# Kernel optimization log

Measured on AMD Instinct MI355X. Metric: run time of the kernel, lower is better.

## Reference

```python
import jax, jax.numpy as jnp
import numpy as np

NL, D, Di, N, R, K, V, NH = 24, 768, 1536, 16, 48, 4, 50280, 12
BATCH, SEQ = 4, 256


def setup_inputs():
    key = jax.random.key(0)
    it = iter(jax.random.split(key, 48))
    g = lambda shape, s=0.02: jax.random.normal(next(it), shape, jnp.float32) * s
    inp = {
        "question_ids": jax.random.randint(next(it), (BATCH, SEQ), 0, V),
        "question_mask": jnp.ones((BATCH, SEQ), jnp.int32),
        "answer_ids": jax.random.randint(next(it), (BATCH, SEQ), 0, V),
        "answer_mask": jnp.ones((BATCH, SEQ), jnp.int32),
        "embed": g((V, D)),
        "norm_w": jnp.ones((NL, D)),
        "in_proj_w": g((NL, 2 * Di, D)),
        "conv_w": g((NL, Di, K), 0.1),
        "conv_b": jnp.zeros((NL, Di)),
        "x_proj_w": g((NL, R + 2 * N, Di)),
        "dt_proj_w": g((NL, Di, R)),
        "dt_proj_b": g((NL, Di), 0.5) - 4.0,
        "A_log": jnp.log(jnp.broadcast_to(jnp.arange(1, N + 1, dtype=jnp.float32), (NL, Di, N))) + 0.0,
        "D_p": jnp.ones((NL, Di)),
        "out_proj_w": g((NL, D, Di)),
        "norm_f": jnp.ones((D,)),
        "ln1_w": jnp.ones((D,)), "ln1_b": jnp.zeros((D,)),
        "qkv_w": g((3 * D, D)), "qkv_b": jnp.zeros((3 * D,)),
        "attn_out_w": g((D, D)), "attn_out_b": jnp.zeros((D,)),
        "ln2_w": jnp.ones((D,)), "ln2_b": jnp.zeros((D,)),
        "ff1_w": g((4 * D, D)), "ff1_b": jnp.zeros((4 * D,)),
        "ff2_w": g((D, 4 * D)), "ff2_b": jnp.zeros((D,)),
        "C_w": g((1, N)), "proj_out_w": g((D, Di)),
        "B_w": g((N, 1)), "proj_in_w": g((Di, D), 0.002),
    }
    return inp


def _rms(x, w, eps=1e-5):
    return x * jax.lax.rsqrt(jnp.mean(x * x, axis=-1, keepdims=True) + eps) * w


def _ln(x, w, b, eps=1e-5):
    m = jnp.mean(x, axis=-1, keepdims=True)
    v = jnp.var(x, axis=-1, keepdims=True)
    return (x - m) * jax.lax.rsqrt(v + eps) * w + b


def _mamba_block(h, layer, init_state):
    nw, ipw, cw, cb, xpw, dpw, dpb, alog, dp, opw = layer
    x_in = _rms(h, nw)
    xz = jnp.einsum('bld,ed->ble', x_in, ipw)  # (B,L,2*Di)
    x, z = jnp.split(xz, 2, axis=-1)
    L = x.shape[1]
    xp = jnp.pad(x, ((0, 0), (K - 1, 0), (0, 0)))  # causal depthwise conv, kernel K
    x = sum(xp[:, k:k + L, :] * cw[:, k] for k in range(K)) + cb
    x = jax.nn.silu(x)
    dbl = jnp.einsum('bld,ed->ble', x, xpw)
    dt, Bm, Cm = dbl[..., :R], dbl[..., R:R + N], dbl[..., R + N:]
    delta = jax.nn.softplus(jnp.einsum('blr,dr->bld', dt, dpw) + dpb)  # (B,L,Di)
    A = -jnp.exp(alog)  # (Di,N)

    def step(hs, t):  # selective scan, carry (B,Di,N)
        d_t, x_t, B_t, C_t = t
        hs = jnp.exp(d_t[..., None] * A) * hs + (d_t * x_t)[..., None] * B_t[:, None, :]
        return hs, jnp.einsum('bdn,bn->bd', hs, C_t)

    xs = tuple(jnp.moveaxis(a, 1, 0) for a in (delta, x, Bm, Cm))
    last, ys = jax.lax.scan(step, init_state, xs)
    y = jnp.moveaxis(ys, 0, 1) + x * dp
    y = y * jax.nn.silu(z)
    return h + jnp.einsum('bld,od->blo', y, opw), last


def _backbone(ids, mask, embed, mamba_params, norm_f, init_states):
    h = embed[ids] * mask[..., None].astype(embed.dtype)
    block = jax.checkpoint(_mamba_block)  # remat per layer: bounds bwd memory

    def layer_step(carry, xs):
        *layer, st = xs
        return block(carry, tuple(layer), st)

    h, lasts = jax.lax.scan(layer_step, h, mamba_params + (init_states,))
    h = _rms(h, norm_f)
    return jnp.einsum('bld,vd->blv', h, embed), lasts  # tied lm head


def _tf_layer(x, ln1_w, ln1_b, qkv_w, qkv_b, attn_out_w, attn_out_b, ln2_w, ln2_b, ff1_w, ff1_b, ff2_w, ff2_b):
    B, S, _ = x.shape
    hd = D // NH
    y = _ln(x, ln1_w, ln1_b)  # norm_first pre-LN
    q, k, v = jnp.split(y @ qkv_w.T + qkv_b, 3, axis=-1)
    q = q.reshape(B, S, NH, hd); k = k.reshape(B, S, NH, hd); v = v.reshape(B, S, NH, hd)
    att = jax.nn.softmax(jnp.einsum('bqhd,bkhd->bhqk', q, k) / jnp.sqrt(jnp.float32(hd)), axis=-1)
    o = jnp.einsum('bhqk,bkhd->bqhd', att, v).reshape(B, S, D)
    x = x + o @ attn_out_w.T + attn_out_b
    y = _ln(x, ln2_w, ln2_b)
    return x + jax.nn.gelu(y @ ff1_w.T + ff1_b, approximate=False) @ ff2_w.T + ff2_b


def _refine(states, C_w, proj_out_w, B_w, proj_in_w, tf_params):
    # states: (B, NL, Di, N); 12-step recurrent state refinement
    for _ in range(12):
        d = jnp.einsum('bsdn,n->bsd', states, C_w[0])  # C: Linear(16,1), squeeze(-1)
        d = jnp.einsum('bsd,od->bso', d, proj_out_w)   # 1536 -> 768
        d = _tf_layer(d, *tf_params)
        d = jnp.einsum('bso,do->bsd', d, proj_in_w)    # 768 -> 1536
        states = states + d[..., None] * B_w[:, 0]     # B: Linear(1,16)
    return states


def reference(question_ids, question_mask, answer_ids, answer_mask, embed, norm_w, in_proj_w, conv_w, conv_b, x_proj_w, dt_proj_w, dt_proj_b, A_log, D_p, out_proj_w, norm_f, ln1_w, ln1_b, qkv_w, qkv_b, attn_out_w, attn_out_b, ln2_w, ln2_b, ff1_w, ff1_b, ff2_w, ff2_b, C_w, proj_out_w, B_w, proj_in_w):
    mamba_params = (norm_w, in_proj_w, conv_w, conv_b, x_proj_w, dt_proj_w, dt_proj_b, A_log, D_p, out_proj_w)
    tf_params = (ln1_w, ln1_b, qkv_w, qkv_b, attn_out_w, attn_out_b, ln2_w, ln2_b, ff1_w, ff1_b, ff2_w, ff2_b)
    Bsz = question_ids.shape[0]
    zeros = jnp.zeros((NL, Bsz, Di, N), embed.dtype)
    _, lasts = _backbone(question_ids, question_mask, embed, mamba_params, norm_f, zeros)
    states = jnp.moveaxis(lasts, 0, 1)  # torch.stack(states, dim=1): (B, NL, Di, N)
    states = _refine(states, C_w, proj_out_w, B_w, proj_in_w, tf_params)
    logits, _ = _backbone(answer_ids, answer_mask, embed, mamba_params, norm_f, jnp.moveaxis(states, 0, 1))
    return logits
```

## Files before the change

### kernel.cpp

```cpp
#include <hip/hip_runtime.h>
#include <math.h>

namespace {

constexpr int kNL = 24, kD = 768, kDi = 1536, kN = 16, kR = 48, kK = 4, kV = 50280, kNH = 12;
constexpr int kB = 4, kS = 256;
constexpr int kMtok = kB * kS;
constexpr int kMref = kB * kNL;
constexpr int kVp = 50304;
constexpr int kKa = 3840;

using bf16x8   = __attribute__((ext_vector_type(8))) short;
using f32x4    = __attribute__((ext_vector_type(4))) float;
using ushort8v = __attribute__((ext_vector_type(8))) unsigned short;

__device__ __forceinline__ float siluf(float x) { return x / (1.f + __expf(-x)); }

__device__ __forceinline__ ushort f2b(float f) {
    union { float f; unsigned u; } v; v.f = f;
    unsigned u = v.u;
    unsigned r = (u + 0x7FFFu + ((u >> 16) & 1u)) >> 16;
    return (ushort)r;
}
__device__ __forceinline__ float b2f(ushort u) {
    union { unsigned u; float f; } v; v.u = (unsigned)u << 16; return v.f;
}

#define GLOAD_LDS(g, l) \
    __builtin_amdgcn_global_load_lds((const __attribute__((address_space(1))) void*)(g), \
                                     (__attribute__((address_space(3))) void*)(l), 16, 0, 0)

template <int BM, int BN, int BIAS, int ACT, int RES, int OUTMODE, int PIPE, int SSQ = 0, int SWZ = 0>
__global__ __launch_bounds__(256, (PIPE == 3 ? 3 : 2)) void gemm_bf16(
    const ushort* __restrict__ A, int lda,
    const ushort* __restrict__ B, int ldb,
    float* __restrict__ C, int ldc,
    ushort* __restrict__ Cbf, int ldcb,
    float* __restrict__ C2,
    const float* __restrict__ bias,
    const float* __restrict__ aux,
    const float* __restrict__ aux2,
    int M, int N, int K)
{
// ... 155 lines not shown
            for (int q = 0; q < 4; ++q) {
                rsq[i][q] += __shfl_xor(rsq[i][q], 1, 16);
                rsq[i][q] += __shfl_xor(rsq[i][q], 2, 16);
                rsq[i][q] += __shfl_xor(rsq[i][q], 4, 16);
                rsq[i][q] += __shfl_xor(rsq[i][q], 8, 16);
            }
        float* red = (float*)&As[0][0];
        __syncthreads();
        if ((lane & 15) == 0) {
#pragma unroll
            for (int i = 0; i < MI; ++i)
#pragma unroll
                for (int q = 0; q < 4; ++q) {
                    int rl = (wave >> 1) * 32 + i * 16 + (lane >> 4) * 4 + q;
                    red[(wave & 1) * 64 + rl] = rsq[i][q];
                }
        }
        __syncthreads();
        if (tid < 64) C2[(size_t)blockIdx.x * kMtok + m0 + tid] = red[tid] + red[64 + tid];
    }
}

template <int BM, int BN, int BIAS, int ACT, int RES, int OUTMODE, int PIPE, int SSQ = 0, int SWZ = 0>
static void gemm(const ushort* A, int lda, const ushort* B, int ldb,
                 float* C, int ldc, ushort* Cb, int ldcb, float* C2,
                 const float* bias, const float* aux, int M, int N, int K, hipStream_t s,
                 const float* aux2 = nullptr)
{
    dim3 g((N + BN - 1) / BN, (M + BM - 1) / BM);
    gemm_bf16<BM, BN, BIAS, ACT, RES, OUTMODE, PIPE, SSQ, SWZ><<<g, dim3(256), 0, s>>>(
        A, lda, B, ldb, C, ldc, Cb, ldcb, C2, bias, aux, aux2, M, N, K);
}

__global__ __launch_bounds__(256, 4) void gemm_rms(
    const float* __restrict__ hbuf, const float* __restrict__ ssq,
    const float* __restrict__ nw,
    const ushort* __restrict__ B, int ldb,
    ushort* __restrict__ Xbf, ushort* __restrict__ zTb,
    int M, int N, int K)
{
    constexpr int MI = 2, NJ = 2, BCH = 2;
    __shared__ ushort As[2][64 * 64];
    __shared__ ushort Bs[2][64 * 64];
    const int tid  = threadIdx.x;
    const int lane = tid & 63;
    const int wave = tid >> 6;
    const int m0 = blockIdx.y * 64;
    const int n0 = blockIdx.x * 64;
    const int wr = (wave >> 1) * 32;
    const int wc = (wave & 1) * 32;

    f32x4 acc[MI][NJ];
#pragma unroll
    for (int i = 0; i < MI; ++i)
#pragma unroll
        for (int j = 0; j < NJ; ++j) acc[i][j] = f32x4{0.f, 0.f, 0.f, 0.f};

    const int srow = lane >> 3;
    const int scol = ((lane & 7) ^ srow) * 8;
    const ushort* gB[BCH];
#pragma unroll
    for (int g = 0; g < BCH; ++g)
        gB[g] = B + (size_t)(n0 + (g * 4 + wave) * 8 + srow) * ldb + scol;

    int arow[2];
    float rs[2];
#pragma unroll
    for (int g = 0; g < 2; ++g) {
        arow[g] = m0 + (g * 4 + wave) * 8 + srow;
        float s = 0.f;
#pragma unroll
        for (int c = 0; c < 12; ++c) s += ssq[c * kMtok + arow[g]];
        rs[g] = rsqrtf(s * (1.f / 768.f) + 1e-5f);
    }

    const int frow = lane & 15;
    const int kh   = lane >> 4;
    const int nt   = K >> 6;

    float4 av[2][2], wv[2];
    auto loadA = [&](int t) {
        int k = t * 64 + scol;
        wv[0] = *(const float4*)&nw[k];
        wv[1] = *(const float4*)&nw[k + 4];
#pragma unroll
        for (int g = 0; g < 2; ++g) {
            av[g][0] = *(const float4*)&hbuf[(size_t)arow[g] * K + k];
            av[g][1] = *(const float4*)&hbuf[(size_t)arow[g] * K + k + 4];
        }
    };
    auto writeA = [&](int buf) {
#pragma unroll
        for (int g = 0; g < 2; ++g) {
            ushort8v o;
            o[0] = f2b(av[g][0].x * rs[g] * wv[0].x);
            o[1] = f2b(av[g][0].y * rs[g] * wv[0].y);
            o[2] = f2b(av[g][0].z * rs[g] * wv[0].z);
            o[3] = f2b(av[g][0].w * rs[g] * wv[0].w);
            o[4] = f2b(av[g][1].x * rs[g] * wv[1].x);
            o[5] = f2b(av[g][1].y * rs[g] * wv[1].y);
            o[6] = f2b(av[g][1].z * rs[g] * wv[1].z);
            o[7] = f2b(av[g][1].w * rs[g] * wv[1].w);
            *(ushort8v*)&As[buf][(g * 4 + wave) * 512 + lane * 8] = o;
        }
    };
    auto stageB = [&](int t, int buf) {
#pragma unroll
        for (int g = 0; g < BCH; ++g) GLOAD_LDS(gB[g] + t * 64, &Bs[buf][(g * 4 + wave) * 512]);
    };
    auto compute = [&](int buf) {
#pragma unroll
        for (int s = 0; s < 2; ++s) {
            bf16x8 fa[MI], fb[NJ];
#pragma unroll
            for (int i = 0; i < MI; ++i) {
                int r = wr + i * 16 + frow;
                int slot = (s * 4 + kh) ^ (r & 7);
                fa[i] = *(const bf16x8*)&As[buf][r * 64 + slot * 8];
            }
#pragma unroll
            for (int j = 0; j < NJ; ++j) {
                int r = wc + j * 16 + frow;
                int slot = (s * 4 + kh) ^ (r & 7);
                fb[j] = *(const bf16x8*)&Bs[buf][r * 64 + slot * 8];
            }
#pragma unroll
            for (int i = 0; i < MI; ++i)
#pragma unroll
                for (int j = 0; j < NJ; ++j)
                    acc[i][j] = __builtin_amdgcn_mfma_f32_16x16x32_bf16(fa[i], fb[j], acc[i][j], 0, 0, 0);
        }
    };

    loadA(0);
    stageB(0, 0);
    writeA(0);
    __syncthreads();
    int cur = 0;
    for (int t = 0; t < nt; ++t) {
        if (t + 1 < nt) { loadA(t + 1); stageB(t + 1, cur ^ 1); }
        compute(cur);
        if (t + 1 < nt) writeA(cur ^ 1);
        __syncthreads();
        cur ^= 1;
    }

    const int ccol = lane & 15;
    const int crow = (lane >> 4) * 4;
#pragma unroll
    for (int i = 0; i < MI; ++i) {
#pragma unroll
        for (int j = 0; j < NJ; ++j) {
            int gn = n0 + wc + j * 16 + ccol;
#pragma unroll
            for (int q = 0; q < 4; ++q) {
                int gm = m0 + wr + i * 16 + crow + q;
                float v = acc[i][j][q];
                if (gn < kDi) Xbf[(size_t)gm * kDi + gn] = f2b(v);
                else zTb[(size_t)(gn - kDi) * kMtok + gm] = f2b(siluf(v));
            }
        }
    }
}

__global__ void cvt_kernel(const float* __restrict__ src, ushort* __restrict__ dst, int n) {
    int i = (blockIdx.x * 256 + threadIdx.x) * 4;
    if (i >= n) return;
    float4 v = *(const float4*)(src + i);
    ushort4 o; o.x = f2b(v.x); o.y = f2b(v.y); o.z = f2b(v.z); o.w = f2b(v.w);
    *(ushort4*)(dst + i) = o;
}

__global__ void cvt_xpw_kernel(const float* __restrict__ src, ushort* __restrict__ dst) {
    int i = (blockIdx.x * 256 + threadIdx.x) * 4;
    if (i >= 24 * 80 * 1536) return;
    int l = i / (80 * 1536), r = i - l * (80 * 1536);
    int row = r / 1536, col = r - row * 1536;
    float4 v = *(const float4*)(src + i);
    ushort4 o; o.x = f2b(v.x); o.y = f2b(v.y); o.z = f2b(v.z); o.w = f2b(v.w);
    *(ushort4*)(dst + ((size_t)(l * 128 + row)) * 1536 + col) = o;
}

__global__ void cvt_dpw_kernel(const float* __restrict__ src, ushort* __restrict__ dst) {
    int i = blockIdx.x * 256 + threadIdx.x;
    if (i >= 24 * 1536 * 64) return;
    int col = i & 63, row = i >> 6;
    dst[i] = (col < 48) ? f2b(src[(size_t)row * 48 + col]) : (ushort)0;
}

__global__ void cvt_ff2T_kernel(const float* __restrict__ src, ushort* __restrict__ dst) {
    int i = blockIdx.x * 256 + threadIdx.x;
    if (i >= 768 * 3072) return;
    int d = i / 3072, f = i - d * 3072;
    dst[(size_t)f * 768 + d] = f2b(src[i]);
}

__global__ void cvt_pi_kernel(const float* __restrict__ src, ushort* __restrict__ dst) {
    int i = blockIdx.x * 256 + threadIdx.x;
    if (i >= 1536 * 768) return;
    int o = i / 768, d = i - o * 768;
    dst[(size_t)o * kKa + d] = f2b(src[i]);
}

__global__ void pib_kernel(const float* __restrict__ piw, const float* __restrict__ ff2b,
                           float* __restrict__ bias2) {
    int o = blockIdx.x * 256 + threadIdx.x;
    if (o >= 1536) return;
    float s = 0.f;
    for (int d = 0; d < 768; ++d) s += piw[(size_t)o * 768 + d] * ff2b[d];
    bias2[o] = s;
}

__global__ void embed_kernel(const int* __restrict__ ids, const int* __restrict__ msk,
                             const float* __restrict__ embed, float* __restrict__ h,
                             float* __restrict__ ssq)
{
    int i = blockIdx.x * 256 + threadIdx.x;
    int row = i / kD, col = i - row * kD;
    float v = embed[(size_t)ids[row] * kD + col] * (float)msk[row];
    h[i] = v;
    float s = v * v;
    s += __shfl_xor(s, 1);  s += __shfl_xor(s, 2);  s += __shfl_xor(s, 4);
    s += __shfl_xor(s, 8);  s += __shfl_xor(s, 16); s += __shfl_xor(s, 32);
    if ((threadIdx.x & 63) == 0) ssq[(col >> 6) * kMtok + row] = s;
}

__global__ __launch_bounds__(256) void rms_kernel(const float* __restrict__ x,
                                                  const float* __restrict__ w,
                                                  ushort* __restrict__ out)
{
    __shared__ float red[256];
    int row = blockIdx.x, tid = threadIdx.x;
    const float* xr = x + (size_t)row * kD;
    float s = 0.f;
    for (int j = tid; j < kD; j += 256) { float v = xr[j]; s += v * v; }
    red[tid] = s; __syncthreads();
    for (int o = 128; o > 0; o >>= 1) { if (tid < o) red[tid] += red[tid + o]; __syncthreads(); }
    float rs = rsqrtf(red[0] / (float)kD + 1e-5f);
    for (int j = tid; j < kD; j += 256) out[(size_t)row * kD + j] = f2b(xr[j] * rs * w[j]);
}

__global__ __launch_bounds__(256) void ln_kernel(const float* __restrict__ x,
                                                 const float* __restrict__ w,
                                                 const float* __restrict__ b,
                                                 ushort* __restrict__ out)
{
    __shared__ float r1[256], r2[256];
    int row = blockIdx.x, tid = threadIdx.x;
    const float* xr = x + (size_t)row * kD;
    float s = 0.f, s2 = 0.f;
    for (int j = tid; j < kD; j += 256) { float v = xr[j]; s += v; s2 += v * v; }
    r1[tid] = s; r2[tid] = s2; __syncthreads();
    for (int o = 128; o > 0; o >>= 1) {
        if (tid < o) { r1[tid] += r1[tid + o]; r2[tid] += r2[tid + o]; }
        __syncthreads();
    }
    float mean = r1[0] / (float)kD;
    float var = r2[0] / (float)kD - mean * mean;
    float rsv = rsqrtf(var + 1e-5f);
    for (int j = tid; j < kD; j += 256)
        out[(size_t)row * kD + j] = f2b((xr[j] - mean) * rsv * w[j] + b[j]);
}

__global__ __launch_bounds__(256) void conv_kernel(
    const ushort* __restrict__ xb, const float* __restrict__ cw,
    const float* __restrict__ cb, ushort* __restrict__ xc_bf,
    ushort* __restrict__ xcT)
{
    int d   = blockIdx.x * 256 + threadIdx.x;
    int bt0 = blockIdx.y * 16;
    int t0  = bt0 & (kS - 1);
    float w0 = cw[d * 4], w1 = cw[d * 4 + 1], w2 = cw[d * 4 + 2], w3 = cw[d * 4 + 3];
    float bias = cb[d];
    float xv[19];
#pragma unroll
    for (int j = 0; j < 19; ++j) {
        int tt = t0 - 3 + j;
        xv[j] = (tt >= 0) ? b2f(xb[(size_t)(bt0 - 3 + j) * kDi + d]) : 0.f;
    }
    ushort8v o0, o1;
#pragma unroll
    for (int e = 0; e < 16; ++e) {
        float s = bias + xv[e] * w0 + xv[e + 1] * w1 + xv[e + 2] * w2 + xv[e + 3] * w3;
        ushort us = f2b(siluf(s));
        xc_bf[(size_t)(bt0 + e) * kDi + d] = us;
        if (e < 8) o0[e] = us; else o1[e - 8] = us;
    }
    *(ushort8v*)(xcT + (size_t)d * kMtok + bt0)     = o0;
    *(ushort8v*)(xcT + (size_t)d * kMtok + bt0 + 8) = o1;
}

__global__ __launch_bounds__(256) void scan_kernel(
    const ushort* __restrict__ dltT, const ushort* __restrict__ xcT,
    const ushort* __restrict__ zT, const float* __restrict__ bcT,
    const float* __restrict__ alog, const float* __restrict__ dp,
    float* __restrict__ states, ushort* __restrict__ y)
{
    int gid = blockIdx.x * 256 + threadIdx.x;
    int n = gid & 15;
    int d = (gid >> 4) % kDi;
    int b = gid / (kDi * kN);
    float Areg = -__expf(alog[d * kN + n]);
    float dpv = dp[d];
    size_t sidx = (size_t)(b * kDi + d) * kN + n;
    float hs = states[sidx];
    const ushort8v* pD = (const ushort8v*)(dltT + (size_t)d * kMtok + b * kS);
    const ushort8v* pX = (const ushort8v*)(xcT  + (size_t)d * kMtok + b * kS);
    const ushort8v* pZ = (const ushort8v*)(zT   + (size_t)d * kMtok + b * kS);
    const float4* pB = (const float4*)(bcT + (size_t)n * kMtok + b * kS);
    const float4* pC = (const float4*)(bcT + (size_t)(16 + n) * kMtok + b * kS);
    ushort8v D = pD[0], X = pX[0], Z = pZ[0];
    float4 B0 = pB[0], B1 = pB[1], C0 = pC[0], C1 = pC[1];
    ushort* yrow = y + (size_t)(b * kS) * kDi + d;
    for (int g = 0; g < kS / 8; ++g) {
        ushort8v Dn, Xn, Zn; float4 Bn0, Bn1, Cn0, Cn1;
        if (g + 1 < kS / 8) {
            Dn = pD[g + 1]; Xn = pX[g + 1]; Zn = pZ[g + 1];
            Bn0 = pB[2 * g + 2]; Bn1 = pB[2 * g + 3];
            Cn0 = pC[2 * g + 2]; Cn1 = pC[2 * g + 3];
        }
#pragma unroll
        for (int e = 0; e < 8; ++e) {
            float dv = b2f(D[e]), xv = b2f(X[e]), zv = b2f(Z[e]);
            float Bv = (e < 4) ? (&B0.x)[e] : (&B1.x)[e - 4];
            float Cv = (e < 4) ? (&C0.x)[e] : (&C1.x)[e - 4];
            hs = __expf(dv * Areg) * hs + (dv * xv) * Bv;
            float p = hs * Cv;
            p += __shfl_xor(p, 1, 16);
            p += __shfl_xor(p, 2, 16);
            p += __shfl_xor(p, 4, 16);
            p += __shfl_xor(p, 8, 16);
            if (n == 0) yrow[(size_t)(g * 8 + e) * kDi] = f2b((p + xv * dpv) * zv);
        }
        D = Dn; X = Xn; Z = Zn; B0 = Bn0; B1 = Bn1; C0 = Cn0; C1 = Cn1;
    }
    states[sidx] = hs;
}

__global__ void contract_kernel(const float* __restrict__ st, const float* __restrict__ Cw,
                                ushort* __restrict__ dDi)
{
    int i = blockIdx.x * 256 + threadIdx.x;
    int row = i / kDi, di = i - row * kDi;
    int b = row / kNL, s = row - b * kNL;
    const float* sp = st + ((size_t)(s * kB + b) * kDi + di) * kN;
    float acc = 0.f;
#pragma unroll
    for (int nn = 0; nn < kN; ++nn) acc += sp[nn] * Cw[nn];
    dDi[i] = f2b(acc);
}

__global__ __launch_bounds__(32) void attn_kernel(const float* __restrict__ qkv,
                                                  ushort* __restrict__ o)
{
    int b = blockIdx.x / kNH;
    int hh = blockIdx.x - b * kNH;
    int sq = threadIdx.x;
    if (sq >= kNL) return;
    const float* qrow = qkv + (size_t)(b * kNL + sq) * (3 * kD) + hh * 64;
    float q[64];
#pragma unroll
    for (int e = 0; e < 64; ++e) q[e] = qrow[e];
    float sc[kNL];
    float mx = -1e30f;
    for (int sk = 0; sk < kNL; ++sk) {
        const float* krow = qkv + (size_t)(b * kNL + sk) * (3 * kD) + kD + hh * 64;
        float dt = 0.f;
#pragma unroll
        for (int e = 0; e < 64; ++e) dt += q[e] * krow[e];
// ... 40 lines not shown
    const float* dpp    = (const float*)d_in[13];
    const float* opw    = (const float*)d_in[14];
    const float* norm_f = (const float*)d_in[15];
    const float* ln1w   = (const float*)d_in[16];
    const float* ln1b   = (const float*)d_in[17];
    const float* qkvw   = (const float*)d_in[18];
    const float* qkvbi  = (const float*)d_in[19];
    const float* aow    = (const float*)d_in[20];
    const float* aob    = (const float*)d_in[21];
    const float* ln2w   = (const float*)d_in[22];
    const float* ln2b   = (const float*)d_in[23];
    const float* ff1w   = (const float*)d_in[24];
    const float* ff1b   = (const float*)d_in[25];
    const float* ff2w   = (const float*)d_in[26];
    const float* ff2b   = (const float*)d_in[27];
    const float* Cwp    = (const float*)d_in[28];
    const float* powp   = (const float*)d_in[29];
    const float* Bwp    = (const float*)d_in[30];
    const float* piwp   = (const float*)d_in[31];

    char* base = (char*)d_ws;
    size_t cur = 0;
    auto allocB = [&](size_t bytes) { char* p = base + cur; cur = (cur + bytes + 255) & ~(size_t)255; return p; };
    auto allocF = [&](size_t n) { return (float*)allocB(n * 4); };
    auto allocH = [&](size_t n) { return (ushort*)allocB(n * 2); };

    float* h     = allocF((size_t)kMtok * kD);
    float* ssqp  = allocF((size_t)12 * kMtok);
    float* bcT   = allocF((size_t)32 * kMtok);
    float* st    = allocF((size_t)kNL * kB * kDi * kN);
    float* x768  = allocF((size_t)kMref * kD);
    float* qkvB  = allocF((size_t)kMref * 3 * kD);
    float* bias2 = allocF((size_t)kDi);
    ushort* x_bf    = allocH((size_t)kMtok * kDi);
    ushort* zT_b    = allocH((size_t)kDi * kMtok);
    ushort* xcT_b   = allocH((size_t)kDi * kMtok);
    ushort* dltT_b  = allocH((size_t)kDi * kMtok);
    ushort* xc_bf   = allocH((size_t)kMtok * kDi);
    ushort* dtin_bf = allocH((size_t)kMtok * 64);
    ushort* yb_bf   = allocH((size_t)kMtok * kDi);
    ushort* xin_bf  = allocH((size_t)kMtok * kD);
    ushort* dDi_bf  = allocH((size_t)128 * kDi);
    ushort* tb_bf   = allocH((size_t)128 * kD);
    ushort* o768_bf = allocH((size_t)128 * kD);
    ushort* A2      = allocH((size_t)128 * kKa);
    ushort* xpw_bf  = allocH((size_t)kNL * 128 * kDi);
    ushort* dpw_bf  = allocH((size_t)kNL * kDi * 64);
    ushort* powp_bf = allocH((size_t)kD * kDi);
    ushort* qkvw_bf = allocH((size_t)3 * kD * kD);
    ushort* aow_bf  = allocH((size_t)kD * kD);
    ushort* ff1w_bf = allocH((size_t)4 * kD * kD);
    ushort* ff2wT   = allocH((size_t)4 * kD * kD);
    ushort* piw_bf  = allocH((size_t)kDi * kD);
    ushort* B2      = allocH((size_t)kDi * kKa);
    ushort* emb_bf  = allocH((size_t)kVp * kD);

    size_t base_end = cur;
    ushort* ipw_all = allocH((size_t)kNL * 2 * kDi * kD);
    ushort* opw_all = allocH((size_t)kNL * kD * kDi);
    bool full = (cur <= ws_size);
    ushort* ipw_stg = nullptr;
    ushort* opw_stg = nullptr;
    if (!full) {
        cur = base_end;
        ipw_stg = allocH((size_t)2 * kDi * kD);
        opw_stg = allocH((size_t)kD * kDi);
        if (cur > ws_size) return;
    }

    auto cvt = [&](const float* s, ushort* d, size_t n) {
        cvt_kernel<<<dim3((unsigned)((n / 4 + 255) / 256)), dim3(256), 0, stream>>>(s, d, (int)n);
    };

    hipMemsetAsync(st, 0, sizeof(float) * (size_t)kNL * kB * kDi * kN, stream);

    cvt_xpw_kernel<<<dim3(2880), dim3(256), 0, stream>>>(xpw, xpw_bf);
    cvt_dpw_kernel<<<dim3(9216), dim3(256), 0, stream>>>(dpw, dpw_bf);
    cvt(powp, powp_bf, (size_t)kD * kDi);
    cvt(qkvw, qkvw_bf, (size_t)3 * kD * kD);
    cvt(aow,  aow_bf,  (size_t)kD * kD);
    cvt(ff1w, ff1w_bf, (size_t)4 * kD * kD);
    cvt(piwp, piw_bf,  (size_t)kDi * kD);
    cvt_ff2T_kernel<<<dim3(9216), dim3(256), 0, stream>>>(ff2w, ff2wT);
    cvt_pi_kernel<<<dim3(4608), dim3(256), 0, stream>>>(piwp, B2);
    pib_kernel<<<dim3(6), dim3(256), 0, stream>>>(piwp, ff2b, bias2);
    gemm<64, 64, 0, 0, 0, 2, 3>(piw_bf, kD, ff2wT, kD, nullptr, 0, B2 + kD, kKa, nullptr,
                                nullptr, nullptr, kDi, 4 * kD, kD, stream);
    cvt(embed, emb_bf, (size_t)kV * kD);
    if (full) {
        cvt(ipw, ipw_all, (size_t)kNL * 2 * kDi * kD);
        cvt(opw, opw_all, (size_t)kNL * kD * kDi);
    }

    for (int pass = 0; pass < 2; ++pass) {
        const int* ids = pass ? a_ids : q_ids;
        const int* msk = pass ? a_msk : q_msk;

        embed_kernel<<<dim3(kMtok * kD / 256), dim3(256), 0, stream>>>(ids, msk, embed, h, ssqp);

        for (int l = 0; l < kNL; ++l) {
            const ushort* ipw_l;
            const ushort* opw_l;
            if (full) {
                ipw_l = ipw_all + (size_t)l * 2 * kDi * kD;
                opw_l = opw_all + (size_t)l * kD * kDi;
            } else {
                cvt(ipw + (size_t)l * 2 * kDi * kD, ipw_stg, (size_t)2 * kDi * kD);
                cvt(opw + (size_t)l * kD * kDi, opw_stg, (size_t)kD * kDi);
                ipw_l = ipw_stg;
                opw_l = opw_stg;
            }
            gemm_rms<<<dim3(48, 16), dim3(256), 0, stream>>>(
                h, ssqp, norm_w + (size_t)l * kD, ipw_l, kD, x_bf, zT_b, kMtok, 2 * kDi, kD);
            conv_kernel<<<dim3(kDi / 256, kMtok / 16), dim3(256), 0, stream>>>(
                x_bf, cw + (size_t)l * kDi * kK, cb + (size_t)l * kDi, xc_bf, xcT_b);
            gemm<64, 64, 0, 0, 0, 3, 3>(xc_bf, kDi, xpw_bf + (size_t)l * 128 * kDi, kDi,
                                        nullptr, 0, dtin_bf, 0, bcT,
                                        nullptr, nullptr, kMtok, 128, kDi, stream);
            gemm<64, 64, 1, 1, 0, 4, 3>(dtin_bf, 64, dpw_bf + (size_t)l * kDi * 64, 64,
                                        nullptr, 0, nullptr, 0, (float*)dltT_b,
                                        dpb + (size_t)l * kDi, nullptr, kMtok, kDi, 64, stream);
            scan_kernel<<<dim3(kB * kDi * kN / 256), dim3(256), 0, stream>>>(
                dltT_b, xcT_b, zT_b, bcT, alog + (size_t)l * kDi * kN, dpp + (size_t)l * kDi,
                st + (size_t)l * kB * kDi * kN, yb_bf);
            if (!(pass == 0 && l == kNL - 1)) {
                gemm<64, 64, 0, 0, 1, 0, 3, 1>(yb_bf, kDi, opw_l, kDi, h, kD, nullptr, 0, ssqp,
                                               nullptr, nullptr, kMtok, kD, kDi, stream);
            }
        }

        if (pass == 0) {
            contract_kernel<<<dim3(kMref * kDi / 256), dim3(256), 0, stream>>>(st, Cwp, dDi_bf);
            for (int it = 0; it < 12; ++it) {
                gemm<64, 64, 0, 0, 0, 0, 3>(dDi_bf, kDi, powp_bf, kDi, x768, kD, nullptr, 0, nullptr,
                                            nullptr, nullptr, kMref, kD, kDi, stream);
                ln_kernel<<<dim3(kMref), dim3(256), 0, stream>>>(x768, ln1w, ln1b, tb_bf);
                gemm<64, 64, 1, 0, 0, 0, 3>(tb_bf, kD, qkvw_bf, kD, qkvB, 3 * kD, nullptr, 0, nullptr,
                                            qkvbi, nullptr, kMref, 3 * kD, kD, stream);
                attn_kernel<<<dim3(kB * kNH), dim3(32), 0, stream>>>(qkvB, o768_bf);
                gemm<64, 64, 1, 0, 1, 1, 3>(o768_bf, kD, aow_bf, kD, x768, kD, A2, kKa, nullptr,
                                            aob, nullptr, kMref, kD, kD, stream);
                ln_kernel<<<dim3(kMref), dim3(256), 0, stream>>>(x768, ln2w, ln2b, tb_bf);
                gemm<64, 64, 1, 2, 0, 2, 3>(tb_bf, kD, ff1w_bf, kD, nullptr, 0, A2 + kD, kKa, nullptr,
                                            ff1b, nullptr, kMref, 4 * kD, kD, stream);
                gemm<64, 64, 1, 0, 0, 7, 3>(A2, kKa, B2, kKa, nullptr, 0, dDi_bf, kDi, st,
                                            bias2, Cwp, kMref, kDi, kKa, stream, Bwp);
            }
        } else {
            rms_kernel<<<dim3(kMtok), dim3(256), 0, stream>>>(h, norm_f, xin_bf);
            gemm<128, 128, 0, 0, 0, 0, 2, 0, 1>(xin_bf, kD, emb_bf, kD, (float*)d_out, kV,
                                                nullptr, 0, nullptr,
                                                nullptr, nullptr, kMtok, kV, kD, stream);
        }
    }
}
```

Baseline: 8.690 ms.

## Fuse the 24-layer Mamba backbone into one persistent kernel with grid barriers

Replaces the per-layer sequence of six kernel launches (rms-gemm, conv, x_proj, dt_proj, scan, out_proj) with a single persistent backbone kernel of 384 blocks. The blocks walk through the stages as device functions and synchronise between stages with a hierarchical atomic grid barrier. The aim is to remove roughly 280 launch gaps and their tail effects per pass. In exchange, each stage is limited to the fixed grid and 2 blocks per CU, and the spin-wait barrier assumes every block is co-resident, which risks deadlock or contention.

```diff
diff --git a/kernel.cpp b/kernel.cpp
--- a/kernel.cpp
+++ b/kernel.cpp
@@ -9,6 +9,7 @@
 constexpr int kMref = kB * kNL;
 constexpr int kVp = 50304;
 constexpr int kKa = 3840;
+constexpr int kNB = 384;
 
 using bf16x8   = __attribute__((ext_vector_type(8))) short;
 using f32x4    = __attribute__((ext_vector_type(4))) float;
@@ -230,36 +231,58 @@
         A, lda, B, ldb, C, ldc, Cb, ldcb, C2, bias, aux, aux2, M, N, K);
 }
 
-__global__ __launch_bounds__(256, 4) void gemm_rms(
-    const float* __restrict__ hbuf, const float* __restrict__ ssq,
-    const float* __restrict__ nw,
-    const ushort* __restrict__ B, int ldb,
-    ushort* __restrict__ Xbf, ushort* __restrict__ zTb,
-    int M, int N, int K)
-{
-    constexpr int MI = 2, NJ = 2, BCH = 2;
-    __shared__ ushort As[2][64 * 64];
-    __shared__ ushort Bs[2][64 * 64];
+
+__device__ __forceinline__ void compute_pair(const ushort* Asb, const ushort* Bsb,
+                                             int wr, int wc, int frow, int kh,
+                                             f32x4 (&acc)[2][2])
+{
+#pragma unroll
+    for (int s = 0; s < 2; ++s) {
+        bf16x8 fa[2], fb[2];
+#pragma unroll
+        for (int i = 0; i < 2; ++i) {
+            int r = wr + i * 16 + frow;
+            int slot = (s * 4 + kh) ^ (r & 7);
+            fa[i] = *(const bf16x8*)&Asb[r * 64 + slot * 8];
+        }
+#pragma unroll
+        for (int j = 0; j < 2; ++j) {
+            int r = wc + j * 16 + frow;
+            int slot = (s * 4 + kh) ^ (r & 7);
+            fb[j] = *(const bf16x8*)&Bsb[r * 64 + slot * 8];
+        }
+#pragma unroll
+        for (int i = 0; i < 2; ++i)
+#pragma unroll
+            for (int j = 0; j < 2; ++j)
+                acc[i][j] = __builtin_amdgcn_mfma_f32_16x16x32_bf16(fa[i], fb[j], acc[i][j], 0, 0, 0);
+    }
+}
+
+__device__ void tile_rms(ushort* As, ushort* Bs,
+    const float* hbuf, const float* ssq, const float* nw,
+    const ushort* Bw, ushort* Xbf, ushort* zTb, int bx, int by)
+{
     const int tid  = threadIdx.x;
     const int lane = tid & 63;
     const int wave = tid >> 6;
-    const int m0 = blockIdx.y * 64;
-    const int n0 = blockIdx.x * 64;
+    const int m0 = by * 64;
+    const int n0 = bx * 64;
     const int wr = (wave >> 1) * 32;
     const int wc = (wave & 1) * 32;
 
-    f32x4 acc[MI][NJ];
-#pragma unroll
-    for (int i = 0; i < MI; ++i)
-#pragma unroll
-        for (int j = 0; j < NJ; ++j) acc[i][j] = f32x4{0.f, 0.f, 0.f, 0.f};
+    f32x4 acc[2][2];
+#pragma unroll
+    for (int i = 0; i < 2; ++i)
+#pragma unroll
+        for (int j = 0; j < 2; ++j) acc[i][j] = f32x4{0.f, 0.f, 0.f, 0.f};
 
     const int srow = lane >> 3;
     const int scol = ((lane & 7) ^ srow) * 8;
-    const ushort* gB[BCH];
-#pragma unroll
-    for (int g = 0; g < BCH; ++g)
-        gB[g] = B + (size_t)(n0 + (g * 4 + wave) * 8 + srow) * ldb + scol;
+    const ushort* gB[2];
+#pragma unroll
+    for (int g = 0; g < 2; ++g)
+        gB[g] = Bw + (size_t)(n0 + (g * 4 + wave) * 8 + srow) * kD + scol;
 
     int arow[2];
     float rs[2];
@@ -274,7 +297,6 @@
 
     const int frow = lane & 15;
     const int kh   = lane >> 4;
-    const int nt   = K >> 6;
 
     float4 av[2][2], wv[2];
     auto loadA = [&](int t) {
@@ -283,8 +305,8 @@
         wv[1] = *(const float4*)&nw[k + 4];
 #pragma unroll
         for (int g = 0; g < 2; ++g) {
-            av[g][0] = *(const float4*)&hbuf[(size_t)arow[g] * K + k];
-            av[g][1] = *(const float4*)&hbuf[(size_t)arow[g] * K + k + 4];
+            av[g][0] = *(const float4*)&hbuf[(size_t)arow[g] * kD + k];
+            av[g][1] = *(const float4*)&hbuf[(size_t)arow[g] * kD + k + 4];
         }
     };
     auto writeA = [&](int buf) {
@@ -299,35 +321,13 @@
             o[5] = f2b(av[g][1].y * rs[g] * wv[1].y);
             o[6] = f2b(av[g][1].z * rs[g] * wv[1].z);
             o[7] = f2b(av[g][1].w * rs[g] * wv[1].w);
-            *(ushort8v*)&As[buf][(g * 4 + wave) * 512 + lane * 8] = o;
+            *(ushort8v*)&As[buf * 4096 + (g * 4 + wave) * 512 + lane * 8] = o;
         }
     };
     auto stageB = [&](int t, int buf) {
 #pragma unroll
-        for (int g = 0; g < BCH; ++g) GLOAD_LDS(gB[g] + t * 64, &Bs[buf][(g * 4 + wave) * 512]);
-    };
-    auto compute = [&](int buf) {
-#pragma unroll
-        for (int s = 0; s < 2; ++s) {
-            bf16x8 fa[MI], fb[NJ];
-#pragma unroll
-            for (int i = 0; i < MI; ++i) {
-                int r = wr + i * 16 + frow;
-                int slot = (s * 4 + kh) ^ (r & 7);
-                fa[i] = *(const bf16x8*)&As[buf][r * 64 + slot * 8];
-            }
-#pragma unroll
-            for (int j = 0; j < NJ; ++j) {
-                int r = wc + j * 16 + frow;
-                int slot = (s * 4 + kh) ^ (r & 7);
-                fb[j] = *(const bf16x8*)&Bs[buf][r * 64 + slot * 8];
-            }
-#pragma unroll
-            for (int i = 0; i < MI; ++i)
-#pragma unroll
-                for (int j = 0; j < NJ; ++j)
-                    acc[i][j] = __builtin_amdgcn_mfma_f32_16x16x32_bf16(fa[i], fb[j], acc[i][j], 0, 0, 0);
-        }
+        for (int g = 0; g < 2; ++g)
+            GLOAD_LDS(gB[g] + t * 64, &Bs[buf * 4096 + (g * 4 + wave) * 512]);
     };
 
     loadA(0);
@@ -335,10 +335,10 @@
     writeA(0);
     __syncthreads();
     int cur = 0;
-    for (int t = 0; t < nt; ++t) {
-        if (t + 1 < nt) { loadA(t + 1); stageB(t + 1, cur ^ 1); }
-        compute(cur);
-        if (t + 1 < nt) writeA(cur ^ 1);
+    for (int t = 0; t < 12; ++t) {
+        if (t + 1 < 12) { loadA(t + 1); stageB(t + 1, cur ^ 1); }
+        compute_pair(As + cur * 4096, Bs + cur * 4096, wr, wc, frow, kh, acc);
+        if (t + 1 < 12) writeA(cur ^ 1);
         __syncthreads();
         cur ^= 1;
     }
@@ -346,9 +346,9 @@
     const int ccol = lane & 15;
     const int crow = (lane >> 4) * 4;
 #pragma unroll
-    for (int i = 0; i < MI; ++i) {
-#pragma unroll
-        for (int j = 0; j < NJ; ++j) {
+    for (int i = 0; i < 2; ++i) {
+#pragma unroll
+        for (int j = 0; j < 2; ++j) {
             int gn = n0 + wc + j * 16 + ccol;
 #pragma unroll
             for (int q = 0; q < 4; ++q) {
@@ -361,112 +361,126 @@
     }
 }
 
-__global__ void cvt_kernel(const float* __restrict__ src, ushort* __restrict__ dst, int n) {
-    int i = (blockIdx.x * 256 + threadIdx.x) * 4;
-    if (i >= n) return;
-    float4 v = *(const float4*)(src + i);
-    ushort4 o; o.x = f2b(v.x); o.y = f2b(v.y); o.z = f2b(v.z); o.w = f2b(v.w);
-    *(ushort4*)(dst + i) = o;
-}
-
-__global__ void cvt_xpw_kernel(const float* __restrict__ src, ushort* __restrict__ dst) {
-    int i = (blockIdx.x * 256 + threadIdx.x) * 4;
-    if (i >= 24 * 80 * 1536) return;
-    int l = i / (80 * 1536), r = i - l * (80 * 1536);
-    int row = r / 1536, col = r - row * 1536;
-    float4 v = *(const float4*)(src + i);
-    ushort4 o; o.x = f2b(v.x); o.y = f2b(v.y); o.z = f2b(v.z); o.w = f2b(v.w);
-    *(ushort4*)(dst + ((size_t)(l * 128 + row)) * 1536 + col) = o;
-}
-
-__global__ void cvt_dpw_kernel(const float* __restrict__ src, ushort* __restrict__ dst) {
-    int i = blockIdx.x * 256 + threadIdx.x;
-    if (i >= 24 * 1536 * 64) return;
-    int col = i & 63, row = i >> 6;
-    dst[i] = (col < 48) ? f2b(src[(size_t)row * 48 + col]) : (ushort)0;
-}
-
-__global__ void cvt_ff2T_kernel(const float* __restrict__ src, ushort* __restrict__ dst) {
-    int i = blockIdx.x * 256 + threadIdx.x;
-    if (i >= 768 * 3072) return;
-    int d = i / 3072, f = i - d * 3072;
-    dst[(size_t)f * 768 + d] = f2b(src[i]);
-}
-
-__global__ void cvt_pi_kernel(const float* __restrict__ src, ushort* __restrict__ dst) {
-    int i = blockIdx.x * 256 + threadIdx.x;
-    if (i >= 1536 * 768) return;
-    int o = i / 768, d = i - o * 768;
-    dst[(size_t)o * kKa + d] = f2b(src[i]);
-}
-
-__global__ void pib_kernel(const float* __restrict__ piw, const float* __restrict__ ff2b,
-                           float* __restrict__ bias2) {
-    int o = blockIdx.x * 256 + threadIdx.x;
-    if (o >= 1536) return;
-    float s = 0.f;
-    for (int d = 0; d < 768; ++d) s += piw[(size_t)o * 768 + d] * ff2b[d];
-    bias2[o] = s;
-}
-
-__global__ void embed_kernel(const int* __restrict__ ids, const int* __restrict__ msk,
-                             const float* __restrict__ embed, float* __restrict__ h,
-                             float* __restrict__ ssq)
-{
-    int i = blockIdx.x * 256 + threadIdx.x;
-    int row = i / kD, col = i - row * kD;
-    float v = embed[(size_t)ids[row] * kD + col] * (float)msk[row];
-    h[i] = v;
-    float s = v * v;
-    s += __shfl_xor(s, 1);  s += __shfl_xor(s, 2);  s += __shfl_xor(s, 4);
-    s += __shfl_xor(s, 8);  s += __shfl_xor(s, 16); s += __shfl_xor(s, 32);
-    if ((threadIdx.x & 63) == 0) ssq[(col >> 6) * kMtok + row] = s;
-}
-
-__global__ __launch_bounds__(256) void rms_kernel(const float* __restrict__ x,
-                                                  const float* __restrict__ w,
-                                                  ushort* __restrict__ out)
-{
-    __shared__ float red[256];
-    int row = blockIdx.x, tid = threadIdx.x;
-    const float* xr = x + (size_t)row * kD;
-    float s = 0.f;
-    for (int j = tid; j < kD; j += 256) { float v = xr[j]; s += v * v; }
-    red[tid] = s; __syncthreads();
-    for (int o = 128; o > 0; o >>= 1) { if (tid < o) red[tid] += red[tid + o]; __syncthreads(); }
-    float rs = rsqrtf(red[0] / (float)kD + 1e-5f);
-    for (int j = tid; j < kD; j += 256) out[(size_t)row * kD + j] = f2b(xr[j] * rs * w[j]);
-}
-
-__global__ __launch_bounds__(256) void ln_kernel(const float* __restrict__ x,
-                                                 const float* __restrict__ w,
-                                                 const float* __restrict__ b,
-                                                 ushort* __restrict__ out)
-{
-    __shared__ float r1[256], r2[256];
-    int row = blockIdx.x, tid = threadIdx.x;
-    const float* xr = x + (size_t)row * kD;
-    float s = 0.f, s2 = 0.f;
-    for (int j = tid; j < kD; j += 256) { float v = xr[j]; s += v; s2 += v * v; }
-    r1[tid] = s; r2[tid] = s2; __syncthreads();
-    for (int o = 128; o > 0; o >>= 1) {
-        if (tid < o) { r1[tid] += r1[tid + o]; r2[tid] += r2[tid + o]; }
+template <int MODE>
+__device__ void tile_gemm(ushort* As, ushort* Bs,
+    const ushort* A, int lda, const ushort* Bw, int ldb,
+    float* C, ushort* Cbf, float* C2, const float* bias,
+    int K, int bx, int by)
+{
+    const int tid  = threadIdx.x;
+    const int lane = tid & 63;
+    const int wave = tid >> 6;
+    const int m0 = by * 64;
+    const int n0 = bx * 64;
+    const int wr = (wave >> 1) * 32;
+    const int wc = (wave & 1) * 32;
+
+    f32x4 acc[2][2];
+#pragma unroll
+    for (int i = 0; i < 2; ++i)
+#pragma unroll
+        for (int j = 0; j < 2; ++j) acc[i][j] = f32x4{0.f, 0.f, 0.f, 0.f};
+
+    const int srow = lane >> 3;
+    const int scol = ((lane & 7) ^ srow) * 8;
+    const ushort* gA[2];
+    const ushort* gB[2];
+#pragma unroll
+    for (int g = 0; g < 2; ++g) {
+        gA[g] = A  + (size_t)(m0 + (g * 4 + wave) * 8 + srow) * lda + scol;
+        gB[g] = Bw + (size_t)(n0 + (g * 4 + wave) * 8 + srow) * ldb + scol;
+    }
+
+    const int frow = lane & 15;
+    const int kh   = lane >> 4;
+    const int nt   = K >> 6;
+
+    auto stage = [&](int t, int buf) {
+        const int off = t * 64;
+#pragma unroll
+        for (int g = 0; g < 2; ++g) {
+            GLOAD_LDS(gA[g] + off, &As[buf * 4096 + (g * 4 + wave) * 512]);
+            GLOAD_LDS(gB[g] + off, &Bs[buf * 4096 + (g * 4 + wave) * 512]);
+        }
+    };
+
+    stage(0, 0);
+    __syncthreads();
+    int cur = 0;
+    for (int t = 0; t < nt; ++t) {
+        if (t + 1 < nt) stage(t + 1, cur ^ 1);
+        compute_pair(As + cur * 4096, Bs + cur * 4096, wr, wc, frow, kh, acc);
         __syncthreads();
-    }
-    float mean = r1[0] / (float)kD;
-    float var = r2[0] / (float)kD - mean * mean;
-    float rsv = rsqrtf(var + 1e-5f);
-    for (int j = tid; j < kD; j += 256)
-        out[(size_t)row * kD + j] = f2b((xr[j] - mean) * rsv * w[j] + b[j]);
-}
-
-__global__ __launch_bounds__(256) void conv_kernel(
-    const ushort* __restrict__ xb, const float* __restrict__ cw,
-    const float* __restrict__ cb, ushort* __restrict__ xc_bf,
-    ushort* __restrict__ xcT)
-{
-    int d   = blockIdx.x * 256 + threadIdx.x;
-    int bt0 = blockIdx.y * 16;
+        cur ^= 1;
+    }
+
+    const int ccol = lane & 15;
+    const int crow = (lane >> 4) * 4;
+    float rsq[2][4];
+    if constexpr (MODE == 0) {
+#pragma unroll
+        for (int i = 0; i < 2; ++i)
+#pragma unroll
+            for (int q = 0; q < 4; ++q) rsq[i][q] = 0.f;
+    }
+#pragma unroll
+    for (int i = 0; i < 2; ++i) {
+#pragma unroll
+        for (int j = 0; j < 2; ++j) {
+            int gn = n0 + wc + j * 16 + ccol;
+#pragma unroll
+            for (int q = 0; q < 4; ++q) {
+                int gm = m0 + wr + i * 16 + crow + q;
+                float v = acc[i][j][q];
+                if constexpr (MODE == 3) {
+                    if (gn < 48) Cbf[(size_t)gm * 64 + gn] = f2b(v);
+                    else if (gn < 64) { Cbf[(size_t)gm * 64 + gn] = 0; C2[(size_t)(gn - 48) * kMtok + gm] = v; }
+                    else if (gn < 80) C2[(size_t)(gn - 48) * kMtok + gm] = v;
+                } else if constexpr (MODE == 4) {
+                    float w = v + bias[gn];
+                    w = fmaxf(w, 0.f) + log1pf(expf(-fabsf(w)));
+                    Cbf[(size_t)gn * kMtok + gm] = f2b(w);
+                } else {
+                    size_t ci = (size_t)gm * kD + gn;
+                    v += C[ci];
+                    C[ci] = v;
+                    rsq[i][q] += v * v;
+                }
+            }
+        }
+    }
+    if constexpr (MODE == 0) {
+#pragma unroll
+        for (int i = 0; i < 2; ++i)
+#pragma unroll
+            for (int q = 0; q < 4; ++q) {
+                rsq[i][q] += __shfl_xor(rsq[i][q], 1, 16);
+                rsq[i][q] += __shfl_xor(rsq[i][q], 2, 16);
+                rsq[i][q] += __shfl_xor(rsq[i][q], 4, 16);
+                rsq[i][q] += __shfl_xor(rsq[i][q], 8, 16);
+            }
+        float* red = (float*)As;
+        __syncthreads();
+        if ((lane & 15) == 0) {
+#pragma unroll
+            for (int i = 0; i < 2; ++i)
+#pragma unroll
+                for (int q = 0; q < 4; ++q) {
+                    int rl = (wave >> 1) * 32 + i * 16 + (lane >> 4) * 4 + q;
+                    red[(wave & 1) * 64 + rl] = rsq[i][q];
+                }
+        }
+        __syncthreads();
+        if (tid < 64) C2[(size_t)bx * kMtok + m0 + tid] = red[tid] + red[64 + tid];
+        __syncthreads();
+    }
+}
+
+__device__ void conv_unit(const ushort* xb, const float* cw, const float* cb,
+                          ushort* xc_bf, ushort* xcT, int bx, int by)
+{
+    int d   = bx * 256 + threadIdx.x;
+    int bt0 = by * 16;
     int t0  = bt0 & (kS - 1);
     float w0 = cw[d * 4], w1 = cw[d * 4 + 1], w2 = cw[d * 4 + 2], w3 = cw[d * 4 + 3];
     float bias = cb[d];
@@ -488,13 +502,11 @@
     *(ushort8v*)(xcT + (size_t)d * kMtok + bt0 + 8) = o1;
 }
 
-__global__ __launch_bounds__(256) void scan_kernel(
-    const ushort* __restrict__ dltT, const ushort* __restrict__ xcT,
-    const ushort* __restrict__ zT, const float* __restrict__ bcT,
-    const float* __restrict__ alog, const float* __restrict__ dp,
-    float* __restrict__ states, ushort* __restrict__ y)
-{
-    int gid = blockIdx.x * 256 + threadIdx.x;
+__device__ void scan_unit(const ushort* dltT, const ushort* xcT, const ushort* zT,
+                          const float* bcT, const float* alog, const float* dp,
+                          float* states, ushort* y, int u)
+{
+    int gid = u * 256 + threadIdx.x;
     int n = gid & 15;
     int d = (gid >> 4) % kDi;
     int b = gid / (kDi * kN);
@@ -533,6 +545,207 @@
         D = Dn; X = Xn; Z = Zn; B0 = Bn0; B1 = Bn1; C0 = Cn0; C1 = Cn1;
     }
     states[sidx] = hs;
+}
+
+__device__ __forceinline__ void gbar(int* leaf, int* root, int* gen)
+{
+    __syncthreads();
+    if (threadIdx.x == 0) {
+        __threadfence();
+        int g = __hip_atomic_load(gen, __ATOMIC_RELAXED, __HIP_MEMORY_SCOPE_AGENT);
+        int a = atomicAdd(&leaf[(blockIdx.x & 63) << 5], 1) + 1;
+        if (a == (g + 1) * (kNB / 64)) {
+            int r = atomicAdd(root, 1) + 1;
+            if (r == (g + 1) * 64)
+                __hip_atomic_fetch_add(gen, 1, __ATOMIC_RELEASE, __HIP_MEMORY_SCOPE_AGENT);
+        }
+        while (__hip_atomic_load(gen, __ATOMIC_ACQUIRE, __HIP_MEMORY_SCOPE_AGENT) == g)
+            __builtin_amdgcn_s_sleep(2);
+        __threadfence();
+    }
+    __syncthreads();
+}
+
+__global__ __launch_bounds__(256, 2) void backbone_kernel(
+    float* h, float* ssqp, const float* norm_w,
+    const ushort* ipw_all, ushort* x_bf, ushort* zT_b,
+    const float* cw, const float* cb, ushort* xc_bf, ushort* xcT_b,
+    const ushort* xpw_bf, ushort* dtin_bf, float* bcT,
+    const ushort* dpw_bf, const float* dpb, ushort* dltT_b,
+    const float* alog, const float* dpp, float* st, ushort* yb_bf,
+    const ushort* opw_all,
+    int* leaf, int* root, int* gen, int pass)
+{
+    __shared__ ushort lds[4 * 4096];
+    ushort* As = lds;
+    ushort* Bs = lds + 2 * 4096;
+    const int nb = gridDim.x;
+
+    for (int l = 0; l < kNL; ++l) {
+        const ushort* ipw_l = ipw_all + (size_t)l * 2 * kDi * kD;
+        const ushort* opw_l = opw_all + (size_t)l * kD * kDi;
+        const ushort* xpw_l = xpw_bf + (size_t)l * 128 * kDi;
+        const ushort* dpw_l = dpw_bf + (size_t)l * kDi * 64;
+        const float* nw_l  = norm_w + (size_t)l * kD;
+        const float* cw_l  = cw + (size_t)l * kDi * kK;
+        const float* cb_l  = cb + (size_t)l * kDi;
+        const float* dpb_l = dpb + (size_t)l * kDi;
+        const float* alog_l = alog + (size_t)l * kDi * kN;
+        const float* dpp_l  = dpp + (size_t)l * kDi;
+        float* st_l = st + (size_t)l * kB * kDi * kN;
+
+        for (int t = blockIdx.x; t < 768; t += nb)
+            tile_rms(As, Bs, h, ssqp, nw_l, ipw_l, x_bf, zT_b, t % 48, t / 48);
+        gbar(leaf, root, gen);
+        for (int u = blockIdx.x; u < 384; u += nb)
+            conv_unit(x_bf, cw_l, cb_l, xc_bf, xcT_b, u % 6, u / 6);
+        gbar(leaf, root, gen);
+        for (int t = blockIdx.x; t < 32; t += nb)
+            tile_gemm<3>(As, Bs, xc_bf, kDi, xpw_l, kDi, nullptr, dtin_bf, bcT, nullptr,
+                         kDi, t % 2, t / 2);
+        gbar(leaf, root, gen);
+        for (int t = blockIdx.x; t < 384; t += nb)
+            tile_gemm<4>(As, Bs, dtin_bf, 64, dpw_l, 64, nullptr, dltT_b, nullptr, dpb_l,
+                         64, t % 24, t / 24);
+        gbar(leaf, root, gen);
+        for (int u = blockIdx.x; u < 384; u += nb)
+            scan_unit(dltT_b, xcT_b, zT_b, bcT, alog_l, dpp_l, st_l, yb_bf, u);
+        gbar(leaf, root, gen);
+        if (!(pass == 0 && l == kNL - 1)) {
+            for (int t = blockIdx.x; t < 192; t += nb)
+                tile_gemm<0>(As, Bs, yb_bf, kDi, opw_l, kDi, h, nullptr, ssqp, nullptr,
+                             kDi, t % 12, t / 12);
+            if (l < kNL - 1) gbar(leaf, root, gen);
+        }
+    }
+}
+
+__global__ __launch_bounds__(256, 4) void gemm_rms(
+    const float* __restrict__ hbuf, const float* __restrict__ ssq,
+    const float* __restrict__ nw,
+    const ushort* __restrict__ B, int ldb,
+    ushort* __restrict__ Xbf, ushort* __restrict__ zTb,
+    int M, int N, int K)
+{
+    __shared__ ushort As[2][64 * 64];
+    __shared__ ushort Bs[2][64 * 64];
+    tile_rms(&As[0][0], &Bs[0][0], hbuf, ssq, nw, B, Xbf, zTb, blockIdx.x, blockIdx.y);
+}
+
+__global__ void conv_kernel(
+    const ushort* __restrict__ xb, const float* __restrict__ cw,
+    const float* __restrict__ cb, ushort* __restrict__ xc_bf,
+    ushort* __restrict__ xcT)
+{
+    conv_unit(xb, cw, cb, xc_bf, xcT, blockIdx.x, blockIdx.y);
+}
+
+__global__ __launch_bounds__(256) void scan_kernel(
+    const ushort* __restrict__ dltT, const ushort* __restrict__ xcT,
+    const ushort* __restrict__ zT, const float* __restrict__ bcT,
+    const float* __restrict__ alog, const float* __restrict__ dp,
+    float* __restrict__ states, ushort* __restrict__ y)
+{
+    scan_unit(dltT, xcT, zT, bcT, alog, dp, states, y, blockIdx.x);
+}
+
+__global__ void cvt_kernel(const float* __restrict__ src, ushort* __restrict__ dst, int n) {
+    int i = (blockIdx.x * 256 + threadIdx.x) * 4;
+    if (i >= n) return;
+    float4 v = *(const float4*)(src + i);
+    ushort4 o; o.x = f2b(v.x); o.y = f2b(v.y); o.z = f2b(v.z); o.w = f2b(v.w);
+    *(ushort4*)(dst + i) = o;
+}
+
+__global__ void cvt_xpw_kernel(const float* __restrict__ src, ushort* __restrict__ dst) {
+    int i = (blockIdx.x * 256 + threadIdx.x) * 4;
+    if (i >= 24 * 80 * 1536) return;
+    int l = i / (80 * 1536), r = i - l * (80 * 1536);
+    int row = r / 1536, col = r - row * 1536;
+    float4 v = *(const float4*)(src + i);
+    ushort4 o; o.x = f2b(v.x); o.y = f2b(v.y); o.z = f2b(v.z); o.w = f2b(v.w);
+    *(ushort4*)(dst + ((size_t)(l * 128 + row)) * 1536 + col) = o;
+}
+
+__global__ void cvt_dpw_kernel(const float* __restrict__ src, ushort* __restrict__ dst) {
+    int i = blockIdx.x * 256 + threadIdx.x;
+    if (i >= 24 * 1536 * 64) return;
+    int col = i & 63, row = i >> 6;
+    dst[i] = (col < 48) ? f2b(src[(size_t)row * 48 + col]) : (ushort)0;
+}
+
+__global__ void cvt_ff2T_kernel(const float* __restrict__ src, ushort* __restrict__ dst) {
+    int i = blockIdx.x * 256 + threadIdx.x;
+    if (i >= 768 * 3072) return;
+    int d = i / 3072, f = i - d * 3072;
+    dst[(size_t)f * 768 + d] = f2b(src[i]);
+}
+
+__global__ void cvt_pi_kernel(const float* __restrict__ src, ushort* __restrict__ dst) {
+    int i = blockIdx.x * 256 + threadIdx.x;
+    if (i >= 1536 * 768) return;
+    int o = i / 768, d = i - o * 768;
+    dst[(size_t)o * kKa + d] = f2b(src[i]);
+}
+
+__global__ void pib_kernel(const float* __restrict__ piw, const float* __restrict__ ff2b,
+                           float* __restrict__ bias2) {
+    int o = blockIdx.x * 256 + threadIdx.x;
+    if (o >= 1536) return;
+    float s = 0.f;
+    for (int d = 0; d < 768; ++d) s += piw[(size_t)o * 768 + d] * ff2b[d];
+    bias2[o] = s;
+}
+
+__global__ void embed_kernel(const int* __restrict__ ids, const int* __restrict__ msk,
+                             const float* __restrict__ embed, float* __restrict__ h,
+                             float* __restrict__ ssq)
+{
+    int i = blockIdx.x * 256 + threadIdx.x;
+    int row = i / kD, col = i - row * kD;
+    float v = embed[(size_t)ids[row] * kD + col] * (float)msk[row];
+    h[i] = v;
+    float s = v * v;
+    s += __shfl_xor(s, 1);  s += __shfl_xor(s, 2);  s += __shfl_xor(s, 4);
+    s += __shfl_xor(s, 8);  s += __shfl_xor(s, 16); s += __shfl_xor(s, 32);
+    if ((threadIdx.x & 63) == 0) ssq[(col >> 6) * kMtok + row] = s;
+}
+
+__global__ __launch_bounds__(256) void rms_kernel(const float* __restrict__ x,
+                                                  const float* __restrict__ w,
+                                                  ushort* __restrict__ out)
+{
+    __shared__ float red[256];
+    int row = blockIdx.x, tid = threadIdx.x;
+    const float* xr = x + (size_t)row * kD;
+    float s = 0.f;
+    for (int j = tid; j < kD; j += 256) { float v = xr[j]; s += v * v; }
+    red[tid] = s; __syncthreads();
+    for (int o = 128; o > 0; o >>= 1) { if (tid < o) red[tid] += red[tid + o]; __syncthreads(); }
+    float rs = rsqrtf(red[0] / (float)kD + 1e-5f);
+    for (int j = tid; j < kD; j += 256) out[(size_t)row * kD + j] = f2b(xr[j] * rs * w[j]);
+}
+
+__global__ __launch_bounds__(256) void ln_kernel(const float* __restrict__ x,
+                                                 const float* __restrict__ w,
+                                                 const float* __restrict__ b,
+                                                 ushort* __restrict__ out)
+{
+    __shared__ float r1[256], r2[256];
+    int row = blockIdx.x, tid = threadIdx.x;
+    const float* xr = x + (size_t)row * kD;
+    float s = 0.f, s2 = 0.f;
+    for (int j = tid; j < kD; j += 256) { float v = xr[j]; s += v; s2 += v * v; }
+    r1[tid] = s; r2[tid] = s2; __syncthreads();
+    for (int o = 128; o > 0; o >>= 1) {
+        if (tid < o) { r1[tid] += r1[tid + o]; r2[tid] += r2[tid + o]; }
+        __syncthreads();
+    }
+    float mean = r1[0] / (float)kD;
+    float var = r2[0] / (float)kD - mean * mean;
+    float rsv = rsqrtf(var + 1e-5f);
+    for (int j = tid; j < kD; j += 256)
+        out[(size_t)row * kD + j] = f2b((xr[j] - mean) * rsv * w[j] + b[j]);
 }
 
 __global__ void contract_kernel(const float* __restrict__ st, const float* __restrict__ Cw,
@@ -639,6 +852,7 @@
     float* x768  = allocF((size_t)kMref * kD);
     float* qkvB  = allocF((size_t)kMref * 3 * kD);
     float* bias2 = allocF((size_t)kDi);
+    int*   barp  = (int*)allocB((2048 + 64) * 4);
     ushort* x_bf    = allocH((size_t)kMtok * kDi);
     ushort* zT_b    = allocH((size_t)kDi * kMtok);
     ushort* xcT_b   = allocH((size_t)kDi * kMtok);
@@ -680,6 +894,7 @@
     };
 
     hipMemsetAsync(st, 0, sizeof(float) * (size_t)kNL * kB * kDi * kN, stream);
+    hipMemsetAsync(barp, 0, (2048 + 64) * 4, stream);
 
     cvt_xpw_kernel<<<dim3(2880), dim3(256), 0, stream>>>(xpw, xpw_bf);
     cvt_dpw_kernel<<<dim3(9216), dim3(256), 0, stream>>>(dpw, dpw_bf);
@@ -699,40 +914,42 @@
         cvt(opw, opw_all, (size_t)kNL * kD * kDi);
     }
 
+    int* leaf = barp;
+    int* root = barp + 2048;
+    int* gen  = barp + 2048 + 32;
+
     for (int pass = 0; pass < 2; ++pass) {
         const int* ids = pass ? a_ids : q_ids;
         const int* msk = pass ? a_msk : q_msk;
 
         embed_kernel<<<dim3(kMtok * kD / 256), dim3(256), 0, stream>>>(ids, msk, embed, h, ssqp);
 
-        for (int l = 0; l < kNL; ++l) {
-            const ushort* ipw_l;
-            const ushort* opw_l;
-            if (full) {
-                ipw_l = ipw_all + (size_t)l * 2 * kDi * kD;
-                opw_l = opw_all + (size_t)l * kD * kDi;
-            } else {
+        if (full) {
+            backbone_kernel<<<dim3(kNB), dim3(256), 0, stream>>>(
+                h, ssqp, norm_w, ipw_all, x_bf, zT_b, cw, cb, xc_bf, xcT_b,
+                xpw_bf, dtin_bf, bcT, dpw_bf, dpb, dltT_b, alog, dpp, st, yb_bf,
+                opw_all, leaf, root, gen, pass);
+        } else {
+            for (int l = 0; l < kNL; ++l) {
                 cvt(ipw + (size_t)l * 2 * kDi * kD, ipw_stg, (size_t)2 * kDi * kD);
                 cvt(opw + (size_t)l * kD * kDi, opw_stg, (size_t)kD * kDi);
-                ipw_l = ipw_stg;
-                opw_l = opw_stg;
-            }
-            gemm_rms<<<dim3(48, 16), dim3(256), 0, stream>>>(
-                h, ssqp, norm_w + (size_t)l * kD, ipw_l, kD, x_bf, zT_b, kMtok, 2 * kDi, kD);
-            conv_kernel<<<dim3(kDi / 256, kMtok / 16), dim3(256), 0, stream>>>(
-                x_bf, cw + (size_t)l * kDi * kK, cb + (size_t)l * kDi, xc_bf, xcT_b);
-            gemm<64, 64, 0, 0, 0, 3, 3>(xc_bf, kDi, xpw_bf + (size_t)l * 128 * kDi, kDi,
-                                        nullptr, 0, dtin_bf, 0, bcT,
-                                        nullptr, nullptr, kMtok, 128, kDi, stream);
-            gemm<64, 64, 1, 1, 0, 4, 3>(dtin_bf, 64, dpw_bf + (size_t)l * kDi * 64, 64,
-                                        nullptr, 0, nullptr, 0, (float*)dltT_b,
-                                        dpb + (size_t)l * kDi, nullptr, kMtok, kDi, 64, stream);
-            scan_kernel<<<dim3(kB * kDi * kN / 256), dim3(256), 0, stream>>>(
-                dltT_b, xcT_b, zT_b, bcT, alog + (size_t)l * kDi * kN, dpp + (size_t)l * kDi,
-                st + (size_t)l * kB * kDi * kN, yb_bf);
-            if (!(pass == 0 && l == kNL - 1)) {
-                gemm<64, 64, 0, 0, 1, 0, 3, 1>(yb_bf, kDi, opw_l, kDi, h, kD, nullptr, 0, ssqp,
-                                               nullptr, nullptr, kMtok, kD, kDi, stream);
+                gemm_rms<<<dim3(48, 16), dim3(256), 0, stream>>>(
+                    h, ssqp, norm_w + (size_t)l * kD, ipw_stg, kD, x_bf, zT_b, kMtok, 2 * kDi, kD);
+                conv_kernel<<<dim3(kDi / 256, kMtok / 16), dim3(256), 0, stream>>>(
+                    x_bf, cw + (size_t)l * kDi * kK, cb + (size_t)l * kDi, xc_bf, xcT_b);
+                gemm<64, 64, 0, 0, 0, 3, 3>(xc_bf, kDi, xpw_bf + (size_t)l * 128 * kDi, kDi,
+                                            nullptr, 0, dtin_bf, 0, bcT,
+                                            nullptr, nullptr, kMtok, 128, kDi, stream);
+                gemm<64, 64, 1, 1, 0, 4, 3>(dtin_bf, 64, dpw_bf + (size_t)l * kDi * 64, 64,
+                                            nullptr, 0, nullptr, 0, (float*)dltT_b,
+                                            dpb + (size_t)l * kDi, nullptr, kMtok, kDi, 64, stream);
+                scan_kernel<<<dim3(kB * kDi * kN / 256), dim3(256), 0, stream>>>(
+                    dltT_b, xcT_b, zT_b, bcT, alog + (size_t)l * kDi * kN, dpp + (size_t)l * kDi,
+                    st + (size_t)l * kB * kDi * kN, yb_bf);
+                if (!(pass == 0 && l == kNL - 1)) {
+                    gemm<64, 64, 0, 0, 1, 0, 3, 1>(yb_bf, kDi, opw_stg, kDi, h, kD, nullptr, 0, ssqp,
+                                                   nullptr, nullptr, kMtok, kD, kDi, stream);
+                }
             }
         }
 
```

New measurement: 24.19 ms. +178.4%, slower.
